# Performance work log

Hardware: AMD Instinct MI355X
Metric: run time of the kernel (lower is better)

The kernel has to match this reference:

```python
import jax, jax.numpy as jnp
import numpy as np

H = 64  # hidden_dim

def _lstm_dir(x, Wih, Whh, bih, bhh, reverse):
    # x: [B, T, D]; Wih: [4H, D]; Whh: [4H, H]; PyTorch gate order i,f,g,o
    B, T, _ = x.shape
    if reverse:
        x = x[:, ::-1, :]
    # Precompute input contribution to all gates: [B, T, 4H]
    xg = jnp.einsum('btd,gd->btg', x, Wih) + (bih + bhh)
    h0 = jnp.zeros((B, H), x.dtype)
    c0 = jnp.zeros((B, H), x.dtype)

    def step(carry, xg_t):
        h, c = carry
        g = xg_t + h @ Whh.T  # [B, 4H]
        i, f, gg, o = jnp.split(g, 4, axis=-1)
        i = jax.nn.sigmoid(i)
        f = jax.nn.sigmoid(f)
        gg = jnp.tanh(gg)
        o = jax.nn.sigmoid(o)
        c = f * c + i * gg
        h = o * jnp.tanh(c)
        return (h, c), h

    (hT, cT), hs = jax.lax.scan(step, (h0, c0), jnp.swapaxes(xg, 0, 1))
    hs = jnp.swapaxes(hs, 0, 1)  # [B, T, H]
    if reverse:
        hs = hs[:, ::-1, :]
    return hs, hT

def _forward(x, Wih_l0_f, Whh_l0_f, bih_l0_f, bhh_l0_f,
             Wih_l0_b, Whh_l0_b, bih_l0_b, bhh_l0_b,
             Wih_l1_f, Whh_l1_f, bih_l1_f, bhh_l1_f,
             Wih_l1_b, Whh_l1_b, bih_l1_b, bhh_l1_b,
             fc1_W, fc1_b, fc2_W, fc2_b):
    xt = jnp.transpose(x, (0, 2, 1))  # [B, 512, 3]
    # Layer 0 (bidirectional)
    hs_f, _ = _lstm_dir(xt, Wih_l0_f, Whh_l0_f, bih_l0_f, bhh_l0_f, False)
    hs_b, _ = _lstm_dir(xt, Wih_l0_b, Whh_l0_b, bih_l0_b, bhh_l0_b, True)
    y0 = jnp.concatenate([hs_f, hs_b], axis=-1)  # [B, 512, 2H]
    # (inter-layer dropout is identity in eval mode)
    # Layer 1 (bidirectional); only final hidden states needed
    _, hT_f = _lstm_dir(y0, Wih_l1_f, Whh_l1_f, bih_l1_f, bhh_l1_f, False)
    _, hT_b = _lstm_dir(y0, Wih_l1_b, Whh_l1_b, bih_l1_b, bhh_l1_b, True)
    h = jnp.concatenate([hT_f, hT_b], axis=-1)  # [B, 2H]
    h = jax.nn.relu(h @ fc1_W.T + fc1_b)
    return h @ fc2_W.T + fc2_b  # [B, num_classes]

def setup_inputs() -> dict:
    key = jax.random.key(0)
    ks = iter(jax.random.split(key, 32))
    B, T, C = 1024, 512, 3
    d = {}
    d['x'] = jax.random.normal(next(ks), (B, C, T), dtype=jnp.float32)
    # PyTorch-style bias init: forget-gate bias = 1, rest 0
    bias = jnp.zeros((4 * H,), jnp.float32).at[H:2 * H].set(1.0)
    for layer, din in [(0, C), (1, 2 * H)]:
        for dirn in ['f', 'b']:
            d[f'Wih_l{layer}_{dirn}'] = jax.random.normal(next(ks), (4 * H, din), dtype=jnp.float32) * 0.1
            d[f'Whh_l{layer}_{dirn}'] = jax.random.normal(next(ks), (4 * H, H), dtype=jnp.float32) * 0.1
            d[f'bih_l{layer}_{dirn}'] = bias
            d[f'bhh_l{layer}_{dirn}'] = jnp.zeros((4 * H,), jnp.float32)
    d['fc1_W'] = jax.random.normal(next(ks), (H, 2 * H), dtype=jnp.float32) * 0.1
    d['fc1_b'] = jnp.zeros((H,), jnp.float32)
    d['fc2_W'] = jax.random.normal(next(ks), (2, H), dtype=jnp.float32) * 0.1
    d['fc2_b'] = jnp.zeros((2,), jnp.float32)
    return d

def reference(x, Wih_l0_f, Whh_l0_f, bih_l0_f, bhh_l0_f,
              Wih_l0_b, Whh_l0_b, bih_l0_b, bhh_l0_b,
              Wih_l1_f, Whh_l1_f, bih_l1_f, bhh_l1_f,
              Wih_l1_b, Whh_l1_b, bih_l1_b, bhh_l1_b,
              fc1_W, fc1_b, fc2_W, fc2_b):
    return _forward(x, Wih_l0_f, Whh_l0_f, bih_l0_f, bhh_l0_f,
                    Wih_l0_b, Whh_l0_b, bih_l0_b, bhh_l0_b,
                    Wih_l1_f, Whh_l1_f, bih_l1_f, bhh_l1_f,
                    Wih_l1_b, Whh_l1_b, bih_l1_b, bhh_l1_b,
                    fc1_W, fc1_b, fc2_W, fc2_b)
```

## Files before the change

kernel.cpp:

```cpp
#include <hip/hip_runtime.h>
#include <stdint.h>

typedef __attribute__((ext_vector_type(8))) short short8;
typedef __attribute__((ext_vector_type(4))) float f32x4;

#define TT 512
#define LSTR 136
#define XS 516

static __device__ __forceinline__ uint32_t f2bf_u(float f){
  union { float f; uint32_t u; } v; v.f = f;
  return (v.u + 0x7fffu + ((v.u >> 16) & 1u)) >> 16;
}
static __device__ __forceinline__ short8 w8f32(const float* p){
  float4 a = *(const float4*)p;
  float4 b = *(const float4*)(p + 4);
  short8 r;
  r[0] = (short)f2bf_u(a.x); r[1] = (short)f2bf_u(a.y);
  r[2] = (short)f2bf_u(a.z); r[3] = (short)f2bf_u(a.w);
  r[4] = (short)f2bf_u(b.x); r[5] = (short)f2bf_u(b.y);
  r[6] = (short)f2bf_u(b.z); r[7] = (short)f2bf_u(b.w);
  return r;
}
static __device__ __forceinline__ float sigx(float x){
  float e = __builtin_amdgcn_exp2f(-1.442695040888963f * x);
  return __builtin_amdgcn_rcpf(1.f + e);
}
static __device__ __forceinline__ float tanhx(float x){
  float e = __builtin_amdgcn_exp2f(-2.885390081777927f * x);
  return fmaf(__builtin_amdgcn_rcpf(1.f + e), 2.f, -1.f);
}
static __device__ __forceinline__ void lds_barrier(){
  asm volatile("s_waitcnt lgkmcnt(0)" ::: "memory");
  __builtin_amdgcn_s_barrier();
}
#define MF(A,B,C) __builtin_amdgcn_mfma_f32_16x16x32_bf16((A),(B),(C),0,0,0)

#define NONLIN_WRITE(A0V, A1V, P1) do { \
    float g0_ = sel0 ? (A0V)[0] : (A1V)[0]; \
    float g1_ = sel0 ? (A0V)[1] : (A1V)[1]; \
    float g2_ = sel0 ? (A0V)[2] : (A1V)[2]; \
    float g3_ = sel0 ? (A0V)[3] : (A1V)[3]; \
    float ii_ = sigx(g0_), ff_ = sigx(g1_), gg_ = tanhx(g2_), oo_ = sigx(g3_); \
    c = fmaf(ff_, c, ii_ * gg_); \
    h = oo_ * tanhx(c); \
    { unsigned short hh_ = (unsigned short)f2bf_u(h); \
      sZ[P1][rw][colw]     = hh_; \
      sZ[P1][rw + 8][colw] = hh_; } \
  } while(0)

__global__ __launch_bounds__(512, 2) void lstm_l0(
    const float* __restrict__ x,
    const float* __restrict__ Wih_f, const float* __restrict__ Whh_f,
    const float* __restrict__ bih_f, const float* __restrict__ bhh_f,
    const float* __restrict__ Wih_b, const float* __restrict__ Whh_b,
    const float* __restrict__ bih_b, const float* __restrict__ bhh_b,
    unsigned short* __restrict__ y0)
{
  const int tid = threadIdx.x;
  const int wv = tid >> 6, lane = tid & 63;
  const int quad = lane >> 4, m16 = lane & 15;
  const int dir = blockIdx.y;
  const int bbase = blockIdx.x * 8;
  const float* Wih = dir ? Wih_b : Wih_f;
  const float* Whh = dir ? Whh_b : Whh_f;
  const float* bih = dir ? bih_b : bih_f;
  const float* bhh = dir ? bhh_b : bhh_f;

  __shared__ __align__(16) unsigned short sZ[2][16][LSTR];
  __shared__ __align__(16) float sX[24 * XS];

  short8 aH[2][2], aX[2];
  f32x4 biasv[2];
  const int gm = (m16 & 3) * 64 + (m16 >> 2);
  #pragma unroll
  for (int i = 0; i < 2; i++){
    const int rt = 2 * wv + i;
    const int g = gm + 4 * rt;
    aH[i][0] = w8f32(Whh + g * 64 + quad * 8);
    aH[i][1] = w8f32(Whh + g * 64 + 32 + quad * 8);
    short8 ax = {0,0,0,0,0,0,0,0};
    if (quad == 0){
      ax[0] = (short)f2bf_u(Wih[g * 3 + 0]);
      ax[1] = (short)f2bf_u(Wih[g * 3 + 1]);
      ax[2] = (short)f2bf_u(Wih[g * 3 + 2]);
    }
    aX[i] = ax;
    const int gu = 4 * rt + quad;
    #pragma unroll
    for (int r = 0; r < 4; r++) biasv[i][r] = bih[r * 64 + gu] + bhh[r * 64 + gu];
  }

  for (int idx = tid; idx < 2 * 16 * LSTR; idx += 512)
    ((unsigned short*)sZ)[idx] = 0;
  for (int i4 = tid; i4 < 3072; i4 += 512){
    const int row = i4 >> 7, t4 = (i4 & 127) * 4;
    *(float4*)&sX[row * XS + t4] = *(const float4*)(x + (size_t)bbase * 1536 + row * 512 + t4);
  }
  __syncthreads();

  const int xrow = 3 * (m16 & 7);
  const bool sel0 = (m16 < 8);
  const int rw = m16 & 7;
  const int colw = 8 * wv + quad + ((m16 >> 3) << 2);
  float c = 0.f, h = 0.f;
  const f32x4 z4 = {0.f, 0.f, 0.f, 0.f};

#define L0STEP(S, P) do { \
    const int t_ = dir ? (TT - 1 - (S)) : (S); \
    short8 b0 = *(const short8*)&sZ[P][m16][     quad * 8]; \
    short8 b1 = *(const short8*)&sZ[P][m16][32 + quad * 8]; \
    short8 bx = {0,0,0,0,0,0,0,0}; \
    if (quad == 0){ \
      bx[0] = (short)f2bf_u(sX[xrow * XS + t_]); \
      bx[1] = (short)f2bf_u(sX[(xrow + 1) * XS + t_]); \
      bx[2] = (short)f2bf_u(sX[(xrow + 2) * XS + t_]); \
    } \
    if (wv == 7 && (S) > 0){ \
      const int tprev = dir ? (TT - (S)) : ((S) - 1); \
      const int br_ = lane >> 3, cc_ = lane & 7; \
      uint4 v_ = *(const uint4*)&sZ[P][br_][cc_ * 8]; \
      *(uint4*)(y0 + ((size_t)(bbase + br_) * TT + tprev) * 128 + dir * 64 + cc_ * 8) = v_; \
    } \
    f32x4 A0 = MF(aH[0][0], b0, biasv[0]); \
    f32x4 A1 = MF(aH[1][0], b0, biasv[1]); \
    A0 = MF(aH[0][1], b1, A0);  A1 = MF(aH[1][1], b1, A1); \
    f32x4 B0 = MF(aX[0], bx, z4); \
    f32x4 B1 = MF(aX[1], bx, z4); \
    f32x4 a0_ = A0 + B0, a1_ = A1 + B1; \
    NONLIN_WRITE(a0_, a1_, (1 - (P))); \
    lds_barrier(); \
  } while(0)

  for (int s = 0; s < TT; s += 2){
    L0STEP(s, 0);
    L0STEP(s + 1, 1);
  }
#undef L0STEP

  if (wv == 7){
    const int tl = dir ? 0 : (TT - 1);
    const int br = lane >> 3, cc = lane & 7;
    uint4 v = *(const uint4*)&sZ[0][br][cc * 8];
    *(uint4*)(y0 + ((size_t)(bbase + br) * TT + tl) * 128 + dir * 64 + cc * 8) = v;
  }
}

__global__ __launch_bounds__(512, 2) void lstm_l1(
    const unsigned short* __restrict__ y0,
    const float* __restrict__ Wih_f, const float* __restrict__ Whh_f,
    const float* __restrict__ bih_f, const float* __restrict__ bhh_f,
    const float* __restrict__ Wih_b, const float* __restrict__ Whh_b,
    const float* __restrict__ bih_b, const float* __restrict__ bhh_b,
    float* __restrict__ hT)
{
  const int tid = threadIdx.x;
  const int wv = tid >> 6, lane = tid & 63;
  const int quad = lane >> 4, m16 = lane & 15;
  const int dir = blockIdx.y;
  const int bbase = blockIdx.x * 8;
  const float* Wih = dir ? Wih_b : Wih_f;
  const float* Whh = dir ? Whh_b : Whh_f;
  const float* bih = dir ? bih_b : bih_f;
  const float* bhh = dir ? bhh_b : bhh_f;

  __shared__ __align__(16) unsigned short sZ[2][16][LSTR];
  __shared__ __align__(16) unsigned short sY[4][8][LSTR];

  short8 aY[2][4], aH[2][2];
  f32x4 biasv[2];
  const int gm = (m16 & 3) * 64 + (m16 >> 2);
  #pragma unroll
  for (int i = 0; i < 2; i++){
    const int rt = 2 * wv + i;
    const int g = gm + 4 * rt;
    #pragma unroll
    for (int kt = 0; kt < 4; kt++) aY[i][kt] = w8f32(Wih + g * 128 + kt * 32 + quad * 8);
    aH[i][0] = w8f32(Whh + g * 64 + quad * 8);
    aH[i][1] = w8f32(Whh + g * 64 + 32 + quad * 8);
    const int gu = 4 * rt + quad;
    #pragma unroll
    for (int r = 0; r < 4; r++) biasv[i][r] = bih[r * 64 + gu] + bhh[r * 64 + gu];
  }

  for (int idx = tid; idx < 2 * 16 * LSTR; idx += 512)
    ((unsigned short*)sZ)[idx] = 0;

  const int srow = tid >> 4, schunk = tid & 15;
  const size_t sgbase = (size_t)(bbase + (srow & 7)) * TT * 128 + schunk * 8;
  float4 hA = make_float4(0.f,0.f,0.f,0.f), hB = make_float4(0.f,0.f,0.f,0.f);
  if (wv < 2){
    const int t0 = dir ? (TT-1) : 0, t1 = dir ? (TT-2) : 1, t2 = dir ? (TT-3) : 2;
    const int t3 = dir ? (TT-4) : 3, t4 = dir ? (TT-5) : 4;
    float4 v0 = *(const float4*)(y0 + sgbase + (size_t)t0 * 128);
    float4 v1 = *(const float4*)(y0 + sgbase + (size_t)t1 * 128);
    float4 v2 = *(const float4*)(y0 + sgbase + (size_t)t2 * 128);
    hA = *(const float4*)(y0 + sgbase + (size_t)t3 * 128);
    hB = *(const float4*)(y0 + sgbase + (size_t)t4 * 128);
    *(float4*)&sY[0][srow][schunk * 8] = v0;
    *(float4*)&sY[1][srow][schunk * 8] = v1;
    *(float4*)&sY[2][srow][schunk * 8] = v2;
  }
  __syncthreads();

  const int m8 = m16 & 7;
  const bool sel0 = (m16 < 8);
  const int rw = m16 & 7;
  const int colw = 8 * wv + quad + ((m16 >> 3) << 2);
  float c = 0.f, h = 0.f;
  const f32x4 z4 = {0.f, 0.f, 0.f, 0.f};

#define L1STEP(S, HOLD) do { \
    const int p = (S) & 1, p1 = p ^ 1, slot = (S) & 3; \
    if (wv < 2){ \
      *(float4*)&sY[((S) + 3) & 3][srow][schunk * 8] = HOLD; \
      int sg = (S) + 5; if (sg > TT - 1) sg = TT - 1; \
      const int tg = dir ? (TT - 1 - sg) : sg; \
      HOLD = *(const float4*)(y0 + sgbase + (size_t)tg * 128); \
    } \
    short8 by0 = *(const short8*)&sY[slot][m8][     quad * 8]; \
    short8 by1 = *(const short8*)&sY[slot][m8][32 + quad * 8]; \
    short8 by2 = *(const short8*)&sY[slot][m8][64 + quad * 8]; \
    short8 by3 = *(const short8*)&sY[slot][m8][96 + quad * 8]; \
    short8 bh0 = *(const short8*)&sZ[p][m16][     quad * 8]; \
    short8 bh1 = *(const short8*)&sZ[p][m16][32 + quad * 8]; \
    f32x4 A0 = MF(aY[0][0], by0, biasv[0]); \
    f32x4 A1 = MF(aY[1][0], by0, biasv[1]); \
    A0 = MF(aY[0][1], by1, A0);  A1 = MF(aY[1][1], by1, A1); \
    f32x4 B0 = MF(aY[0][2], by2, z4); \
    f32x4 B1 = MF(aY[1][2], by2, z4); \
    B0 = MF(aY[0][3], by3, B0);  B1 = MF(aY[1][3], by3, B1); \
    A0 = MF(aH[0][0], bh0, A0);  A1 = MF(aH[1][0], bh0, A1); \
    B0 = MF(aH[0][1], bh1, B0);  B1 = MF(aH[1][1], bh1, B1); \
    f32x4 a0_ = A0 + B0, a1_ = A1 + B1; \
    NONLIN_WRITE(a0_, a1_, p1); \
    if ((S) == TT - 1){ \
      hT[(size_t)(bbase + rw) * 128 + dir * 64 + colw] = h; \
    } \
    lds_barrier(); \
  } while(0)

  for (int s = 0; s < TT; s += 2){
    L1STEP(s, hA);
    L1STEP(s + 1, hB);
  }
#undef L1STEP
}

__global__ __launch_bounds__(256, 1) void fc_kernel(
    const float* __restrict__ hT,
    const float* __restrict__ w1, const float* __restrict__ b1,
    const float* __restrict__ w2, const float* __restrict__ b2,
    float* __restrict__ out)
{
  __shared__ float sh[4][64];
  const int wave = threadIdx.x >> 6, lane = threadIdx.x & 63;
  const int b = blockIdx.x * 4 + wave;
  float acc = b1[lane];
  const float* hrow = hT + (size_t)b * 128;
  #pragma unroll
  for (int k = 0; k < 128; k += 4){
    float4 h4 = *(const float4*)(hrow + k);
    float4 w4 = *(const float4*)(w1 + lane * 128 + k);
    acc = fmaf(w4.x, h4.x, acc);
    acc = fmaf(w4.y, h4.y, acc);
    acc = fmaf(w4.z, h4.z, acc);
    acc = fmaf(w4.w, h4.w, acc);
  }
  sh[wave][lane] = fmaxf(acc, 0.f);
  __syncthreads();
  if (lane < 2){
    float a = b2[lane];
    #pragma unroll
    for (int k = 0; k < 64; k++) a = fmaf(w2[lane * 64 + k], sh[wave][k], a);
    out[(size_t)b * 2 + lane] = a;
  }
}

extern "C" void kernel_launch(void* const* d_in, const int* in_sizes, int n_in,
                              void* d_out, int out_size, void* d_ws, size_t ws_size,
                              hipStream_t stream){
  (void)in_sizes; (void)n_in; (void)out_size; (void)ws_size;
  const float* x     = (const float*)d_in[0];
  const float* Wih0f = (const float*)d_in[1];
  const float* Whh0f = (const float*)d_in[2];
  const float* bih0f = (const float*)d_in[3];
  const float* bhh0f = (const float*)d_in[4];
  const float* Wih0b = (const float*)d_in[5];
  const float* Whh0b = (const float*)d_in[6];
  const float* bih0b = (const float*)d_in[7];
  const float* bhh0b = (const float*)d_in[8];
  const float* Wih1f = (const float*)d_in[9];
  const float* Whh1f = (const float*)d_in[10];
  const float* bih1f = (const float*)d_in[11];
  const float* bhh1f = (const float*)d_in[12];
  const float* Wih1b = (const float*)d_in[13];
  const float* Whh1b = (const float*)d_in[14];
  const float* bih1b = (const float*)d_in[15];
  const float* bhh1b = (const float*)d_in[16];
  const float* fc1W  = (const float*)d_in[17];
  const float* fc1b  = (const float*)d_in[18];
  const float* fc2W  = (const float*)d_in[19];
  const float* fc2b  = (const float*)d_in[20];
  float* out = (float*)d_out;

  unsigned short* y0 = (unsigned short*)d_ws;
  float* hT = (float*)((char*)d_ws + (size_t)1024 * TT * 128 * 2);

  dim3 grid(128, 2), block(512);
  lstm_l0<<<grid, block, 0, stream>>>(x, Wih0f, Whh0f, bih0f, bhh0f,
                                      Wih0b, Whh0b, bih0b, bhh0b, y0);
  lstm_l1<<<grid, block, 0, stream>>>(y0, Wih1f, Whh1f, bih1f, bhh1f,
                                      Wih1b, Whh1b, bih1b, bhh1b, hT);
  fc_kernel<<<dim3(256), dim3(256), 0, stream>>>(hT, fc1W, fc1b, fc2W, fc2b, out);
}
```

Before: 566.1 us.

## Hoist input-gate MFMAs off the recurrent critical path and spread staging across waves

Both LSTM layers now compute the next timestep's input contribution (x or y0 projection plus bias) after the current nonlinearity write, so each step's critical path holds only the two recurrent h·Whh MFMAs before the activations. A sched_barrier keeps the compiler from moving this precompute back ahead of the recurrent chain. The y0 store in layer 0 and the prefetch staging in layer 1 move from one or two dedicated waves to a few lanes in every wave, spreading the memory traffic evenly. The cost is extra live accumulator registers and a changed instruction order that could affect occupancy or latency hiding.

New measurement: 560.4 us. About the same (-1.0%).

```diff
diff --git a/kernel.cpp b/kernel.cpp
--- a/kernel.cpp
+++ b/kernel.cpp
@@ -104,31 +104,46 @@
   const int rw = m16 & 7;
   const int colw = 8 * wv + quad + ((m16 >> 3) << 2);
   float c = 0.f, h = 0.f;
-  const f32x4 z4 = {0.f, 0.f, 0.f, 0.f};
+
+  f32x4 FB0, FB1;
+  {
+    const int t0_ = dir ? (TT - 1) : 0;
+    short8 bx = {0,0,0,0,0,0,0,0};
+    if (quad == 0){
+      bx[0] = (short)f2bf_u(sX[xrow * XS + t0_]);
+      bx[1] = (short)f2bf_u(sX[(xrow + 1) * XS + t0_]);
+      bx[2] = (short)f2bf_u(sX[(xrow + 2) * XS + t0_]);
+    }
+    FB0 = MF(aX[0], bx, biasv[0]);
+    FB1 = MF(aX[1], bx, biasv[1]);
+  }
 
 #define L0STEP(S, P) do { \
-    const int t_ = dir ? (TT - 1 - (S)) : (S); \
-    short8 b0 = *(const short8*)&sZ[P][m16][     quad * 8]; \
-    short8 b1 = *(const short8*)&sZ[P][m16][32 + quad * 8]; \
-    short8 bx = {0,0,0,0,0,0,0,0}; \
-    if (quad == 0){ \
-      bx[0] = (short)f2bf_u(sX[xrow * XS + t_]); \
-      bx[1] = (short)f2bf_u(sX[(xrow + 1) * XS + t_]); \
-      bx[2] = (short)f2bf_u(sX[(xrow + 2) * XS + t_]); \
-    } \
-    if (wv == 7 && (S) > 0){ \
+    const int p1_ = (P) ^ 1; \
+    short8 bh0 = *(const short8*)&sZ[P][m16][     quad * 8]; \
+    short8 bh1 = *(const short8*)&sZ[P][m16][32 + quad * 8]; \
+    if (lane < 8 && (S) > 0){ \
       const int tprev = dir ? (TT - (S)) : ((S) - 1); \
-      const int br_ = lane >> 3, cc_ = lane & 7; \
-      uint4 v_ = *(const uint4*)&sZ[P][br_][cc_ * 8]; \
-      *(uint4*)(y0 + ((size_t)(bbase + br_) * TT + tprev) * 128 + dir * 64 + cc_ * 8) = v_; \
-    } \
-    f32x4 A0 = MF(aH[0][0], b0, biasv[0]); \
-    f32x4 A1 = MF(aH[1][0], b0, biasv[1]); \
-    A0 = MF(aH[0][1], b1, A0);  A1 = MF(aH[1][1], b1, A1); \
-    f32x4 B0 = MF(aX[0], bx, z4); \
-    f32x4 B1 = MF(aX[1], bx, z4); \
-    f32x4 a0_ = A0 + B0, a1_ = A1 + B1; \
-    NONLIN_WRITE(a0_, a1_, (1 - (P))); \
+      uint4 v_ = *(const uint4*)&sZ[P][wv][lane * 8]; \
+      *(uint4*)(y0 + ((size_t)(bbase + wv) * TT + tprev) * 128 + dir * 64 + lane * 8) = v_; \
+    } \
+    f32x4 A0 = MF(aH[0][0], bh0, FB0); \
+    f32x4 A1 = MF(aH[1][0], bh0, FB1); \
+    A0 = MF(aH[0][1], bh1, A0); \
+    A1 = MF(aH[1][1], bh1, A1); \
+    NONLIN_WRITE(A0, A1, p1_); \
+    { int sn_ = (S) + 1; if (sn_ > TT - 1) sn_ = TT - 1; \
+      const int tn_ = dir ? (TT - 1 - sn_) : sn_; \
+      short8 bx = {0,0,0,0,0,0,0,0}; \
+      if (quad == 0){ \
+        bx[0] = (short)f2bf_u(sX[xrow * XS + tn_]); \
+        bx[1] = (short)f2bf_u(sX[(xrow + 1) * XS + tn_]); \
+        bx[2] = (short)f2bf_u(sX[(xrow + 2) * XS + tn_]); \
+      } \
+      FB0 = MF(aX[0], bx, biasv[0]); \
+      FB1 = MF(aX[1], bx, biasv[1]); \
+    } \
+    __builtin_amdgcn_sched_barrier(0); \
     lds_barrier(); \
   } while(0)
 
@@ -138,11 +153,10 @@
   }
 #undef L0STEP
 
-  if (wv == 7){
+  if (lane < 8){
     const int tl = dir ? 0 : (TT - 1);
-    const int br = lane >> 3, cc = lane & 7;
-    uint4 v = *(const uint4*)&sZ[0][br][cc * 8];
-    *(uint4*)(y0 + ((size_t)(bbase + br) * TT + tl) * 128 + dir * 64 + cc * 8) = v;
+    uint4 v = *(const uint4*)&sZ[0][wv][lane * 8];
+    *(uint4*)(y0 + ((size_t)(bbase + wv) * TT + tl) * 128 + dir * 64 + lane * 8) = v;
   }
 }
 
@@ -186,10 +200,10 @@
   for (int idx = tid; idx < 2 * 16 * LSTR; idx += 512)
     ((unsigned short*)sZ)[idx] = 0;
 
-  const int srow = tid >> 4, schunk = tid & 15;
-  const size_t sgbase = (size_t)(bbase + (srow & 7)) * TT * 128 + schunk * 8;
+  const bool stager = (lane < 16);
+  const size_t sgbase = (size_t)(bbase + wv) * TT * 128 + (size_t)lane * 8;
   float4 hA = make_float4(0.f,0.f,0.f,0.f), hB = make_float4(0.f,0.f,0.f,0.f);
-  if (wv < 2){
+  if (stager){
     const int t0 = dir ? (TT-1) : 0, t1 = dir ? (TT-2) : 1, t2 = dir ? (TT-3) : 2;
     const int t3 = dir ? (TT-4) : 3, t4 = dir ? (TT-5) : 4;
     float4 v0 = *(const float4*)(y0 + sgbase + (size_t)t0 * 128);
@@ -197,9 +211,9 @@
     float4 v2 = *(const float4*)(y0 + sgbase + (size_t)t2 * 128);
     hA = *(const float4*)(y0 + sgbase + (size_t)t3 * 128);
     hB = *(const float4*)(y0 + sgbase + (size_t)t4 * 128);
-    *(float4*)&sY[0][srow][schunk * 8] = v0;
-    *(float4*)&sY[1][srow][schunk * 8] = v1;
-    *(float4*)&sY[2][srow][schunk * 8] = v2;
+    *(float4*)&sY[0][wv][lane * 8] = v0;
+    *(float4*)&sY[1][wv][lane * 8] = v1;
+    *(float4*)&sY[2][wv][lane * 8] = v2;
   }
   __syncthreads();
 
@@ -208,41 +222,56 @@
   const int rw = m16 & 7;
   const int colw = 8 * wv + quad + ((m16 >> 3) << 2);
   float c = 0.f, h = 0.f;
-  const f32x4 z4 = {0.f, 0.f, 0.f, 0.f};
-
-#define L1STEP(S, HOLD) do { \
-    const int p = (S) & 1, p1 = p ^ 1, slot = (S) & 3; \
-    if (wv < 2){ \
-      *(float4*)&sY[((S) + 3) & 3][srow][schunk * 8] = HOLD; \
-      int sg = (S) + 5; if (sg > TT - 1) sg = TT - 1; \
-      const int tg = dir ? (TT - 1 - sg) : sg; \
-      HOLD = *(const float4*)(y0 + sgbase + (size_t)tg * 128); \
-    } \
-    short8 by0 = *(const short8*)&sY[slot][m8][     quad * 8]; \
-    short8 by1 = *(const short8*)&sY[slot][m8][32 + quad * 8]; \
-    short8 by2 = *(const short8*)&sY[slot][m8][64 + quad * 8]; \
-    short8 by3 = *(const short8*)&sY[slot][m8][96 + quad * 8]; \
-    short8 bh0 = *(const short8*)&sZ[p][m16][     quad * 8]; \
-    short8 bh1 = *(const short8*)&sZ[p][m16][32 + quad * 8]; \
-    f32x4 A0 = MF(aY[0][0], by0, biasv[0]); \
-    f32x4 A1 = MF(aY[1][0], by0, biasv[1]); \
-    A0 = MF(aY[0][1], by1, A0);  A1 = MF(aY[1][1], by1, A1); \
-    f32x4 B0 = MF(aY[0][2], by2, z4); \
-    f32x4 B1 = MF(aY[1][2], by2, z4); \
-    B0 = MF(aY[0][3], by3, B0);  B1 = MF(aY[1][3], by3, B1); \
-    A0 = MF(aH[0][0], bh0, A0);  A1 = MF(aH[1][0], bh0, A1); \
-    B0 = MF(aH[0][1], bh1, B0);  B1 = MF(aH[1][1], bh1, B1); \
-    f32x4 a0_ = A0 + B0, a1_ = A1 + B1; \
-    NONLIN_WRITE(a0_, a1_, p1); \
+
+  f32x4 FB0, FB1;
+  {
+    short8 by0 = *(const short8*)&sY[0][m8][     quad * 8];
+    short8 by1 = *(const short8*)&sY[0][m8][32 + quad * 8];
+    short8 by2 = *(const short8*)&sY[0][m8][64 + quad * 8];
+    short8 by3 = *(const short8*)&sY[0][m8][96 + quad * 8];
+    FB0 = MF(aY[0][0], by0, biasv[0]);
+    FB1 = MF(aY[1][0], by0, biasv[1]);
+    FB0 = MF(aY[0][1], by1, FB0);  FB1 = MF(aY[1][1], by1, FB1);
+    FB0 = MF(aY[0][2], by2, FB0);  FB1 = MF(aY[1][2], by2, FB1);
+    FB0 = MF(aY[0][3], by3, FB0);  FB1 = MF(aY[1][3], by3, FB1);
+  }
+
+#define L1STEP(S, P, HOLD) do { \
+    const int p1_ = (P) ^ 1; \
+    short8 bh0 = *(const short8*)&sZ[P][m16][     quad * 8]; \
+    short8 bh1 = *(const short8*)&sZ[P][m16][32 + quad * 8]; \
+    f32x4 A0 = MF(aH[0][0], bh0, FB0); \
+    f32x4 A1 = MF(aH[1][0], bh0, FB1); \
+    A0 = MF(aH[0][1], bh1, A0); \
+    A1 = MF(aH[1][1], bh1, A1); \
+    NONLIN_WRITE(A0, A1, p1_); \
     if ((S) == TT - 1){ \
       hT[(size_t)(bbase + rw) * 128 + dir * 64 + colw] = h; \
     } \
+    if (stager){ \
+      *(float4*)&sY[((S) + 3) & 3][wv][lane * 8] = HOLD; \
+      int sg_ = (S) + 5; if (sg_ > TT - 1) sg_ = TT - 1; \
+      const int tg_ = dir ? (TT - 1 - sg_) : sg_; \
+      HOLD = *(const float4*)(y0 + sgbase + (size_t)tg_ * 128); \
+    } \
+    { const int sl_ = ((S) + 1) & 3; \
+      short8 by0 = *(const short8*)&sY[sl_][m8][     quad * 8]; \
+      short8 by1 = *(const short8*)&sY[sl_][m8][32 + quad * 8]; \
+      short8 by2 = *(const short8*)&sY[sl_][m8][64 + quad * 8]; \
+      short8 by3 = *(const short8*)&sY[sl_][m8][96 + quad * 8]; \
+      FB0 = MF(aY[0][0], by0, biasv[0]); \
+      FB1 = MF(aY[1][0], by0, biasv[1]); \
+      FB0 = MF(aY[0][1], by1, FB0);  FB1 = MF(aY[1][1], by1, FB1); \
+      FB0 = MF(aY[0][2], by2, FB0);  FB1 = MF(aY[1][2], by2, FB1); \
+      FB0 = MF(aY[0][3], by3, FB0);  FB1 = MF(aY[1][3], by3, FB1); \
+    } \
+    __builtin_amdgcn_sched_barrier(0); \
     lds_barrier(); \
   } while(0)
 
   for (int s = 0; s < TT; s += 2){
-    L1STEP(s, hA);
-    L1STEP(s + 1, hB);
+    L1STEP(s, 0, hA);
+    L1STEP(s + 1, 1, hB);
   }
 #undef L1STEP
 }
```
